# Kernel tuning notes

Measured on AMD Instinct MI355X. Metric: run time of the kernel, lower is better.

Reference implementation:

```python
import jax, jax.numpy as jnp
import numpy as np

N = 50000
E = 800000
D_IN = 128
D_HID = 128
D_OUT = 64
BN_EPS = 1e-5


def setup_inputs() -> dict:
    key = jax.random.key(0)
    ks = jax.random.split(key, 8)
    x = jax.random.normal(ks[0], (N, D_IN), dtype=jnp.float32)
    edge_index = jax.random.randint(ks[1], (2, E), 0, N, dtype=jnp.int64)
    # fc1
    W1 = jax.random.normal(ks[2], (D_IN, D_HID), dtype=jnp.float32) / np.sqrt(D_IN)
    b1 = jnp.zeros((D_HID,), dtype=jnp.float32)
    # bn1 affine params
    gamma = jnp.ones((D_HID,), dtype=jnp.float32)
    beta = jnp.zeros((D_HID,), dtype=jnp.float32)
    # fc2
    W2 = jax.random.normal(ks[3], (D_HID, D_OUT), dtype=jnp.float32) / np.sqrt(D_HID)
    b2 = jnp.zeros((D_OUT,), dtype=jnp.float32)
    return {"x": x, "W1": W1, "b1": b1, "gamma": gamma, "beta": beta,
            "W2": W2, "b2": b2, "edge_index": edge_index}


def _propagate(x, row, col):
    # add self loops for every node (reference convention)
    n = x.shape[0]
    sl = jnp.arange(n, dtype=row.dtype)
    row_f = jnp.concatenate([row, sl])
    col_f = jnp.concatenate([col, sl])
    # symmetric degree normalization: deg computed over destinations (col)
    deg = jax.ops.segment_sum(jnp.ones_like(col_f, dtype=x.dtype), col_f, num_segments=n)
    dis = deg ** -0.5
    w = dis[col_f] * dis[row_f]                       # [E+N]
    msg = w[:, None] * x[row_f]                       # [E+N, D] gather + scale
    return jax.ops.segment_sum(msg, col_f, num_segments=n)  # scatter-add


def reference(x, W1, b1, gamma, beta, W2, b2, edge_index):
    row, col = edge_index[0], edge_index[1]
    h = x @ W1 + b1                                   # [N, D_HID]
    h = _propagate(h, row, col)
    # BatchNorm1d with batch statistics (training-mode math, deterministic)
    mu = jnp.mean(h, axis=0)
    var = jnp.var(h, axis=0)
    h = (h - mu) * jax.lax.rsqrt(var + BN_EPS) * gamma + beta
    h = jax.nn.relu(h)
    # dropout treated as identity (eval) for a deterministic reference
    h = h @ W2 + b2                                   # [N, D_OUT]
    h = _propagate(h, row, col)
    return jax.nn.log_softmax(h, axis=1)
```

## Files before the change

### kernel.cpp

```cpp
#include <hip/hip_runtime.h>
#include <hip/hip_bf16.h>

#define N_NODES 50000
#define NE      800000
#define DIN     128
#define DHID    128
#define DOUT    64
#define BN_EPS  1e-5f
#define SLOT    64
#define NBUK    196
#define BCAP    4864
#define EPB     2048
#define NPART   32
#define LDW     132
#define LDW2    132

typedef __hip_bfloat16 bf16;
typedef short bf16x8 __attribute__((ext_vector_type(8)));
typedef float f32x4 __attribute__((ext_vector_type(4)));

__device__ __forceinline__ float ldf(const void* p, int i, int isbf) {
    if (isbf) return __bfloat162float(((const bf16*)p)[i]);
    return ((const float*)p)[i];
}
__device__ __forceinline__ unsigned short f2b(float f) {
    bf16 h = __float2bfloat16(f);
    return *(unsigned short*)&h;
}
__device__ __forceinline__ float2 up2(unsigned int u) {
    return make_float2(__uint_as_float(u << 16), __uint_as_float(u & 0xffff0000u));
}
__device__ __forceinline__ unsigned int pk2(float a, float b) {
    return ((unsigned int)f2b(a)) | (((unsigned int)f2b(b)) << 16);
}

#define DETECT_ISBF(W1raw, tid, sdet, isbf_out)                                   \
    if ((tid) == 0) sdet = 0;                                                     \
    __syncthreads();                                                              \
    {                                                                             \
        unsigned int u_ = ((unsigned int)((const unsigned short*)(W1raw))[tid]) << 16; \
        float f_ = fabsf(__uint_as_float(u_));                                    \
        if (!isnan(f_) && !isinf(f_) && f_ > 1e4f) atomicOr(&sdet, 1);            \
    }                                                                             \
    __syncthreads();                                                              \
    const int isbf_out = !sdet;

__global__ __launch_bounds__(256) void k_binA(const void* eiraw, int* __restrict__ gcnt,
                                              unsigned int* __restrict__ bpk) {
    __shared__ int hist4[4][256];
    __shared__ int cur4[4][256];
    __shared__ int eofs[256], gbase[256];
    __shared__ int wsum[4];
    __shared__ unsigned int stg[EPB];
    __shared__ int sdet;
    int tid = threadIdx.x;
    int lane = tid & 63;
    int wv = tid >> 6;
    if (tid == 0) sdet = 0;
    #pragma unroll
    for (int w2 = 0; w2 < 4; ++w2) hist4[w2][tid] = 0;
    __syncthreads();
    if (tid < 64 && ((const unsigned int*)eiraw)[2 * tid + 1] != 0u) atomicOr(&sdet, 1);
    __syncthreads();
    const int isll = !sdet;

    int e0 = blockIdx.x * EPB;
    int nE = NE - e0; if (nE > EPB) nE = EPB;
    int r[8], c[8];
    #pragma unroll
    for (int q = 0; q < 8; ++q) {
        int li = q * 256 + tid;
        if (li < nE) {
            int e = e0 + li;
            if (isll) { r[q] = (int)((const long long*)eiraw)[e]; c[q] = (int)((const long long*)eiraw)[NE + e]; }
            else      { r[q] = ((const int*)eiraw)[e];            c[q] = ((const int*)eiraw)[NE + e]; }
            atomicAdd(&hist4[wv][c[q] >> 8], 1);
        } else r[q] = -1;
    }
    __syncthreads();
    int h0 = hist4[0][tid], h1 = hist4[1][tid], h2 = hist4[2][tid], h3 = hist4[3][tid];
    int tot = h0 + h1 + h2 + h3;
    int inc = tot;
    #pragma unroll
    for (int off = 1; off < 64; off <<= 1) {
        int u = __shfl_up(inc, off, 64);
        if (lane >= off) inc += u;
    }
    if (lane == 63) wsum[wv] = inc;
    __syncthreads();
    int woff = 0;
    #pragma unroll
    for (int w2 = 0; w2 < 3; ++w2) if (w2 < wv) woff += wsum[w2];
    int ex = woff + inc - tot;
    eofs[tid] = ex;
    cur4[0][tid] = ex;
    cur4[1][tid] = ex + h0;
    cur4[2][tid] = ex + h0 + h1;
    cur4[3][tid] = ex + h0 + h1 + h2;
    if (tid < NBUK) gbase[tid] = atomicAdd(&gcnt[tid], tot);
    __syncthreads();
    #pragma unroll
    for (int q = 0; q < 8; ++q) {
        if (r[q] >= 0) {
            int b = c[q] >> 8;
            int p = atomicAdd(&cur4[wv][b], 1);
            stg[p] = ((unsigned int)b << 24) | ((unsigned int)(c[q] & 255) << 16) | (unsigned int)r[q];
        }
    }
    __syncthreads();
    for (int i = tid; i < nE; i += 256) {
        unsigned int v = stg[i];
        int b = v >> 24;
        int pos = gbase[b] + (i - eofs[b]);
        if (pos < BCAP) bpk[(size_t)b * BCAP + pos] = v;
    }
}

__global__ __launch_bounds__(256) void k_binB(const unsigned int* __restrict__ bpk, const int* __restrict__ gcnt,
                                              int* __restrict__ counts, int* __restrict__ ej) {
    __shared__ int cnt4[4][256];
    __shared__ int cur4[4][256];
    __shared__ int eofs[256];
    __shared__ int wsum[4];
    __shared__ unsigned int stg[BCAP];
    int b = blockIdx.x;
    int tid = threadIdx.x;
    int lane = tid & 63;
    int wv = tid >> 6;
    int m = gcnt[b]; if (m > BCAP) m = BCAP;
    #pragma unroll
    for (int w2 = 0; w2 < 4; ++w2) cnt4[w2][tid] = 0;
    __syncthreads();
    const unsigned int* src = bpk + (size_t)b * BCAP;
    for (int i = tid; i < m; i += 256)
        atomicAdd(&cnt4[wv][(src[i] >> 16) & 255], 1);
    __syncthreads();
    int h0 = cnt4[0][tid], h1 = cnt4[1][tid], h2 = cnt4[2][tid], h3 = cnt4[3][tid];
    int hv = h0 + h1 + h2 + h3;
    int inc = hv;
    #pragma unroll
    for (int off = 1; off < 64; off <<= 1) {
        int u = __shfl_up(inc, off, 64);
        if (lane >= off) inc += u;
    }
    if (lane == 63) wsum[wv] = inc;
    __syncthreads();
    int woff = 0;
    #pragma unroll
    for (int w2 = 0; w2 < 3; ++w2) if (w2 < wv) woff += wsum[w2];
    int ex = woff + inc - hv;
    eofs[tid] = ex;
    cur4[0][tid] = ex;
    cur4[1][tid] = ex + h0;
    cur4[2][tid] = ex + h0 + h1;
    cur4[3][tid] = ex + h0 + h1 + h2;
    int c0 = b << 8;
    int cg = c0 + tid;
    if (cg < N_NODES) {
        counts[cg] = hv;
        int hc = hv < SLOT ? hv : SLOT;
        int hp = (hc + 15) & ~15; if (hp > SLOT) hp = SLOT;
        for (int k = hc; k < hp; ++k) ej[(size_t)cg * SLOT + k] = N_NODES;
    }
    __syncthreads();
    for (int i = tid; i < m; i += 256) {
        unsigned int v = src[i];
        int cl = (v >> 16) & 255;
        int p = atomicAdd(&cur4[wv][cl], 1);
        stg[p] = v & 0x00ffffffu;
    }
    __syncthreads();
    for (int i = tid; i < m; i += 256) {
        unsigned int v = stg[i];
        int cl = v >> 16;
        int k = i - eofs[cl];
        if (k < SLOT) ej[(size_t)(c0 + cl) * SLOT + k] = (int)(v & 0xffffu);
    }
}

__global__ __launch_bounds__(256) void k_gemm1_mfma(const void* __restrict__ x, const void* __restrict__ W1,
                                                    const void* __restrict__ b1, const int* __restrict__ counts,
                                                    unsigned short* __restrict__ g1) {
    __shared__ unsigned short wt[128 * LDW];
    __shared__ int sdet;
    int tid = threadIdx.x;
    DETECT_ISBF(W1, tid, sdet, isbf)

    #pragma unroll 4
    for (int i = 0; i < 64; ++i) {
        int idx = i * 256 + tid;
        int k = idx >> 7, n = idx & 127;
        wt[n * LDW + k] = isbf ? ((const unsigned short*)W1)[idx]
                               : f2b(((const float*)W1)[idx]);
    }
    __syncthreads();

    int lane = tid & 63;
    int wave = tid >> 6;
    int m0 = blockIdx.x * 64 + wave * 16;
    int lm = lane & 15;
    int quad = lane >> 4;

    bf16x8 a[4];
    int arow = m0 + lm;
    int arow_c = arow < N_NODES ? arow : 0;
    if (isbf) {
        const unsigned short* xb = (const unsigned short*)x;
        #pragma unroll
        for (int q = 0; q < 4; ++q)
            a[q] = *(const bf16x8*)(xb + arow_c * DIN + q * 32 + quad * 8);
    } else {
        const float* xf = (const float*)x;
        #pragma unroll
        for (int q = 0; q < 4; ++q) {
            bf16x8 t;
            #pragma unroll
            for (int j = 0; j < 8; ++j)
                t[j] = (short)f2b(xf[arow_c * DIN + q * 32 + quad * 8 + j]);
            a[q] = t;
        }
    }

    float dsc[4];
    #pragma unroll
    for (int r = 0; r < 4; ++r) {
        int grow = m0 + quad * 4 + r;
        dsc[r] = (grow < N_NODES) ? rsqrtf((float)(counts[grow] + 1)) : 0.f;
    }

    #pragma unroll
    for (int nt = 0; nt < 8; ++nt) {
        int n0 = nt * 16;
        f32x4 acc = {0.f, 0.f, 0.f, 0.f};
        #pragma unroll
        for (int q = 0; q < 4; ++q) {
            bf16x8 b = *(const bf16x8*)(wt + (n0 + lm) * LDW + q * 32 + quad * 8);
            acc = __builtin_amdgcn_mfma_f32_16x16x32_bf16(a[q], b, acc, 0, 0, 0);
        }
        float bias = ldf(b1, n0 + lm, isbf);
        #pragma unroll
        for (int r = 0; r < 4; ++r) {
            int grow = m0 + quad * 4 + r;
            if (grow <= N_NODES)
                g1[grow * DHID + n0 + lm] = f2b(dsc[r] * (acc[r] + bias));
        }
    }
}

__global__ __launch_bounds__(256) void k_prop1(const int* __restrict__ counts, const int* __restrict__ ej,
                                               const unsigned int* __restrict__ g1p,
                                               unsigned int* __restrict__ agg1p,
                                               float* __restrict__ statsP) {
    __shared__ float sp[1024];
    int tid = threadIdx.x;
    int w = tid >> 6;
    int n = blockIdx.x * 4 + w;
    n = __builtin_amdgcn_readfirstlane(n);
    int lane = tid & 63;
    float ax = 0.f, ay = 0.f;
    if (n < N_NODES) {
        int cnt = counts[n];
        int t = cnt < SLOT ? cnt : SLOT;
        int tp = (t + 15) & ~15; if (tp > SLOT) tp = SLOT;
        const int* ejn = ej + (size_t)n * SLOT;
        float2 v = up2(g1p[(size_t)n * 64 + lane]);
        float ax0 = v.x, ay0 = v.y, ax1 = 0.f, ay1 = 0.f;
        float ax2 = 0.f, ay2 = 0.f, ax3 = 0.f, ay3 = 0.f;
        for (int j = 0; j < tp; j += 16) {
            const int4* ej4 = (const int4*)(ejn + j);
            int4 E0 = ej4[0], E1 = ej4[1], E2 = ej4[2], E3 = ej4[3];
            int e[16] = {E0.x, E0.y, E0.z, E0.w, E1.x, E1.y, E1.z, E1.w,
                         E2.x, E2.y, E2.z, E2.w, E3.x, E3.y, E3.z, E3.w};
            unsigned int gg[16];
            #pragma unroll
            for (int q = 0; q < 16; ++q) gg[q] = g1p[(size_t)e[q] * 64 + lane];
            #pragma unroll
            for (int q = 0; q < 16; ++q) {
                float2 f = up2(gg[q]);
                if ((q & 3) == 0) { ax0 += f.x; ay0 += f.y; }
                else if ((q & 3) == 1) { ax1 += f.x; ay1 += f.y; }
                else if ((q & 3) == 2) { ax2 += f.x; ay2 += f.y; }
                else { ax3 += f.x; ay3 += f.y; }
            }
        }
        float dv = rsqrtf((float)(cnt + 1));
        ax = dv * ((ax0 + ax1) + (ax2 + ax3));
        ay = dv * ((ay0 + ay1) + (ay2 + ay3));
        agg1p[(size_t)n * 64 + lane] = pk2(ax, ay);
    }
    sp[w * 256 + 2 * lane]       = ax;
    sp[w * 256 + 2 * lane + 1]   = ay;
    sp[w * 256 + 128 + 2 * lane] = ax * ax;
    sp[w * 256 + 129 + 2 * lane] = ay * ay;
    __syncthreads();
    float s = sp[tid] + sp[256 + tid] + sp[512 + tid] + sp[768 + tid];
    atomicAdd(&statsP[(blockIdx.x & (NPART - 1)) * 256 + tid], s);
}

__global__ __launch_bounds__(256) void k_gemm2_mfma(const unsigned int* __restrict__ agg1p,
                                                    const float* __restrict__ statsP,
                                                    const void* __restrict__ gamma, const void* __restrict__ beta,
                                                    const void* __restrict__ W2, const void* __restrict__ b2,
                                                    const void* __restrict__ W1, const int* __restrict__ counts,
                                                    unsigned short* __restrict__ g2) {
    __shared__ unsigned short w2t[64 * LDW2];
    __shared__ float sc[128], sh[128], redu[256];
    __shared__ int sdet;
    int tid = threadIdx.x;
    DETECT_ISBF(W1, tid, sdet, isbf)

    #pragma unroll 4
    for (int i = 0; i < 32; ++i) {
        int idx = i * 256 + tid;
        int k = idx >> 6, n = idx & 63;
        w2t[n * LDW2 + k] = isbf ? ((const unsigned short*)W2)[idx]
                                 : f2b(((const float*)W2)[idx]);
    }
    {
        float s = 0.f;
        #pragma unroll
        for (int p = 0; p < NPART; ++p) s += statsP[p * 256 + tid];
        redu[tid] = s;
    }
    __syncthreads();
    if (tid < 128) {
        const float invn = 1.0f / (float)N_NODES;
        float mu = redu[tid] * invn;
        float var = redu[128 + tid] * invn - mu * mu;
        float rs = rsqrtf(var + BN_EPS);
        float g = ldf(gamma, tid, isbf);
        sc[tid] = rs * g;
        sh[tid] = ldf(beta, tid, isbf) - mu * rs * g;
    }
    __syncthreads();

    int lane = tid & 63;
    int wave = tid >> 6;
    int m0 = blockIdx.x * 64 + wave * 16;
    int lm = lane & 15;
    int quad = lane >> 4;

    int arow = m0 + lm;
    int arow_c = arow < N_NODES ? arow : 0;
    bf16x8 a[4];
    #pragma unroll
    for (int q = 0; q < 4; ++q) {
        uint4 gv = *(const uint4*)(agg1p + (size_t)arow_c * 64 + q * 16 + quad * 4);
        int kb = q * 32 + quad * 8;
        float2 f0 = up2(gv.x), f1 = up2(gv.y), f2 = up2(gv.z), f3 = up2(gv.w);
        float e0 = f0.x * sc[kb + 0] + sh[kb + 0];
        float e1 = f0.y * sc[kb + 1] + sh[kb + 1];
        float e2 = f1.x * sc[kb + 2] + sh[kb + 2];
        float e3 = f1.y * sc[kb + 3] + sh[kb + 3];
        float e4 = f2.x * sc[kb + 4] + sh[kb + 4];
        float e5 = f2.y * sc[kb + 5] + sh[kb + 5];
        float e6 = f3.x * sc[kb + 6] + sh[kb + 6];
        float e7 = f3.y * sc[kb + 7] + sh[kb + 7];
        bf16x8 t;
        t[0] = (short)f2b(e0 > 0.f ? e0 : 0.f);
        t[1] = (short)f2b(e1 > 0.f ? e1 : 0.f);
        t[2] = (short)f2b(e2 > 0.f ? e2 : 0.f);
        t[3] = (short)f2b(e3 > 0.f ? e3 : 0.f);
        t[4] = (short)f2b(e4 > 0.f ? e4 : 0.f);
        t[5] = (short)f2b(e5 > 0.f ? e5 : 0.f);
        t[6] = (short)f2b(e6 > 0.f ? e6 : 0.f);
        t[7] = (short)f2b(e7 > 0.f ? e7 : 0.f);
        a[q] = t;
    }

    float dsc[4];
    #pragma unroll
    for (int r = 0; r < 4; ++r) {
        int grow = m0 + quad * 4 + r;
        dsc[r] = (grow < N_NODES) ? rsqrtf((float)(counts[grow] + 1)) : 0.f;
    }

    #pragma unroll
    for (int nt = 0; nt < 4; ++nt) {
        int n0 = nt * 16;
        f32x4 acc = {0.f, 0.f, 0.f, 0.f};
        #pragma unroll
        for (int q = 0; q < 4; ++q) {
            bf16x8 b = *(const bf16x8*)(w2t + (n0 + lm) * LDW2 + q * 32 + quad * 8);
            acc = __builtin_amdgcn_mfma_f32_16x16x32_bf16(a[q], b, acc, 0, 0, 0);
        }
        float bias = ldf(b2, n0 + lm, isbf);
        #pragma unroll
        for (int r = 0; r < 4; ++r) {
            int grow = m0 + quad * 4 + r;
            if (grow <= N_NODES)
                g2[grow * DOUT + n0 + lm] = f2b(dsc[r] * (acc[r] + bias));
        }
    }
}

__global__ __launch_bounds__(256) void k_prop2_lsm(const int* __restrict__ counts, const int* __restrict__ ej,
                                                   const unsigned int* __restrict__ g2p,
                                                   const void* __restrict__ W1, void* __restrict__ out) {
    __shared__ int sdet;
    int tid = threadIdx.x;
    DETECT_ISBF(W1, tid, sdet, isbf)

    int n = blockIdx.x * 8 + (tid >> 5);
    if (n >= N_NODES) return;
    int lane = tid & 31;
    int cnt = counts[n];
    int t = cnt < SLOT ? cnt : SLOT;
    int tp = (t + 15) & ~15; if (tp > SLOT) tp = SLOT;
    const int* ejn = ej + (size_t)n * SLOT;
    float2 v = up2(g2p[(size_t)n * 32 + lane]);
    float ax0 = v.x, ay0 = v.y, ax1 = 0.f, ay1 = 0.f;
    float ax2 = 0.f, ay2 = 0.f, ax3 = 0.f, ay3 = 0.f;
    for (int j = 0; j < tp; j += 16) {
        const int4* ej4 = (const int4*)(ejn + j);
        int4 E0 = ej4[0], E1 = ej4[1], E2 = ej4[2], E3 = ej4[3];
        int e[16] = {E0.x, E0.y, E0.z, E0.w, E1.x, E1.y, E1.z, E1.w,
                     E2.x, E2.y, E2.z, E2.w, E3.x, E3.y, E3.z, E3.w};
        unsigned int gg[16];
        #pragma unroll
        for (int q = 0; q < 16; ++q) gg[q] = g2p[(size_t)e[q] * 32 + lane];
        #pragma unroll
        for (int q = 0; q < 16; ++q) {
            float2 f = up2(gg[q]);
            if ((q & 3) == 0) { ax0 += f.x; ay0 += f.y; }
            else if ((q & 3) == 1) { ax1 += f.x; ay1 += f.y; }
            else if ((q & 3) == 2) { ax2 += f.x; ay2 += f.y; }
            else { ax3 += f.x; ay3 += f.y; }
        }
    }
    float dv = rsqrtf((float)(cnt + 1));
    float ax = dv * ((ax0 + ax1) + (ax2 + ax3));
    float ay = dv * ((ay0 + ay1) + (ay2 + ay3));
    float m = fmaxf(ax, ay);
    #pragma unroll
    for (int off = 16; off >= 1; off >>= 1) m = fmaxf(m, __shfl_xor(m, off, 32));
    float sum = __expf(ax - m) + __expf(ay - m);
    #pragma unroll
    for (int off = 16; off >= 1; off >>= 1) sum += __shfl_xor(sum, off, 32);
    float lse = m + __logf(sum);
    float rx = ax - lse, ry = ay - lse;
    if (isbf) {
        ((unsigned int*)out)[(size_t)n * 32 + lane] = pk2(rx, ry);
    } else {
        float2* o = (float2*)((float*)out + (size_t)n * 64 + 2 * lane);
        *o = make_float2(rx, ry);
    }
}

extern "C" void kernel_launch(void* const* d_in, const int* in_sizes, int n_in,
                              void* d_out, int out_size, void* d_ws, size_t ws_size,
                              hipStream_t stream) {
    const void* x     = d_in[0];
    const void* W1    = d_in[1];
    const void* b1    = d_in[2];
    const void* gamma = d_in[3];
    const void* beta  = d_in[4];
    const void* W2    = d_in[5];
    const void* b2    = d_in[6];
    const void* ei    = d_in[7];

    char* w = (char*)d_ws;
    float*          statsP = (float*)(w + 0);
    int*            gcnt   = (int*)(w + 32768);
    int*            counts = (int*)(w + 33792);
    int*            ej     = (int*)(w + 233792);
    unsigned int*   bpk    = (unsigned int*)(w + 13033792);
    unsigned short* g1     = (unsigned short*)(w + 16847168);
    unsigned int*   agg1p  = (unsigned int*)(w + 29647424);
    unsigned short* g2     = (unsigned short*)(w + 42447424);

    hipMemsetAsync(w, 0, 33792, stream);

    k_binA<<<(NE + EPB - 1) / EPB, 256, 0, stream>>>(ei, gcnt, bpk);
    k_binB<<<NBUK, 256, 0, stream>>>(bpk, gcnt, counts, ej);

    k_gemm1_mfma<<<(N_NODES + 63) / 64, 256, 0, stream>>>(x, W1, b1, counts, g1);

    k_prop1<<<(N_NODES + 3) / 4, 256, 0, stream>>>(counts, ej, (const unsigned int*)g1, agg1p, statsP);

    k_gemm2_mfma<<<(N_NODES + 63) / 64, 256, 0, stream>>>(agg1p, statsP, gamma, beta, W2, b2,
                                                          W1, counts, g2);

    k_prop2_lsm<<<(N_NODES + 7) / 8, 256, 0, stream>>>(counts, ej, (const unsigned int*)g2, W1, d_out);
}
```

Before: 216.9 us.

## Merge binning and first GEMM into one launch, apply source normalization in prop1

The bucket-sort second pass and the first MFMA GEMM now run as separate block ranges of a single kernel. This is possible because the GEMM no longer multiplies by the source degree normalization. That scaling moves into the first propagation, which gathers a per-node rsqrt(deg) array written by the binning blocks. The goal is to drop one launch and the dependency between binning and GEMM1 so both can overlap. The cost is an extra 4-byte gather per edge in prop1, and GEMM blocks must now wait behind the larger shared-memory footprint.

After: 213.8 us. No clear change (-1.5%).

```diff
diff --git a/kernel.cpp b/kernel.cpp
--- a/kernel.cpp
+++ b/kernel.cpp
@@ -14,6 +14,7 @@
 #define NPART   32
 #define LDW     132
 #define LDW2    132
+#define G1_BLOCKS ((N_NODES + 63) / 64)
 
 typedef __hip_bfloat16 bf16;
 typedef short bf16x8 __attribute__((ext_vector_type(8)));
@@ -116,138 +117,143 @@
     }
 }
 
-__global__ __launch_bounds__(256) void k_binB(const unsigned int* __restrict__ bpk, const int* __restrict__ gcnt,
-                                              int* __restrict__ counts, int* __restrict__ ej) {
-    __shared__ int cnt4[4][256];
-    __shared__ int cur4[4][256];
-    __shared__ int eofs[256];
-    __shared__ int wsum[4];
-    __shared__ unsigned int stg[BCAP];
-    int b = blockIdx.x;
-    int tid = threadIdx.x;
-    int lane = tid & 63;
-    int wv = tid >> 6;
-    int m = gcnt[b]; if (m > BCAP) m = BCAP;
-    #pragma unroll
-    for (int w2 = 0; w2 < 4; ++w2) cnt4[w2][tid] = 0;
-    __syncthreads();
-    const unsigned int* src = bpk + (size_t)b * BCAP;
-    for (int i = tid; i < m; i += 256)
-        atomicAdd(&cnt4[wv][(src[i] >> 16) & 255], 1);
-    __syncthreads();
-    int h0 = cnt4[0][tid], h1 = cnt4[1][tid], h2 = cnt4[2][tid], h3 = cnt4[3][tid];
-    int hv = h0 + h1 + h2 + h3;
-    int inc = hv;
-    #pragma unroll
-    for (int off = 1; off < 64; off <<= 1) {
-        int u = __shfl_up(inc, off, 64);
-        if (lane >= off) inc += u;
-    }
-    if (lane == 63) wsum[wv] = inc;
-    __syncthreads();
-    int woff = 0;
-    #pragma unroll
-    for (int w2 = 0; w2 < 3; ++w2) if (w2 < wv) woff += wsum[w2];
-    int ex = woff + inc - hv;
-    eofs[tid] = ex;
-    cur4[0][tid] = ex;
-    cur4[1][tid] = ex + h0;
-    cur4[2][tid] = ex + h0 + h1;
-    cur4[3][tid] = ex + h0 + h1 + h2;
-    int c0 = b << 8;
-    int cg = c0 + tid;
-    if (cg < N_NODES) {
-        counts[cg] = hv;
-        int hc = hv < SLOT ? hv : SLOT;
-        int hp = (hc + 15) & ~15; if (hp > SLOT) hp = SLOT;
-        for (int k = hc; k < hp; ++k) ej[(size_t)cg * SLOT + k] = N_NODES;
-    }
-    __syncthreads();
-    for (int i = tid; i < m; i += 256) {
-        unsigned int v = src[i];
-        int cl = (v >> 16) & 255;
-        int p = atomicAdd(&cur4[wv][cl], 1);
-        stg[p] = v & 0x00ffffffu;
-    }
-    __syncthreads();
-    for (int i = tid; i < m; i += 256) {
-        unsigned int v = stg[i];
-        int cl = v >> 16;
-        int k = i - eofs[cl];
-        if (k < SLOT) ej[(size_t)(c0 + cl) * SLOT + k] = (int)(v & 0xffffu);
-    }
-}
-
-__global__ __launch_bounds__(256) void k_gemm1_mfma(const void* __restrict__ x, const void* __restrict__ W1,
-                                                    const void* __restrict__ b1, const int* __restrict__ counts,
+__global__ __launch_bounds__(256) void k_binB_gemm1(const unsigned int* __restrict__ bpk,
+                                                    const int* __restrict__ gcnt,
+                                                    int* __restrict__ counts, float* __restrict__ disv,
+                                                    int* __restrict__ ej,
+                                                    const void* __restrict__ x, const void* __restrict__ W1,
+                                                    const void* __restrict__ b1,
                                                     unsigned short* __restrict__ g1) {
-    __shared__ unsigned short wt[128 * LDW];
+    __shared__ __align__(16) char smraw[33792];
     __shared__ int sdet;
     int tid = threadIdx.x;
-    DETECT_ISBF(W1, tid, sdet, isbf)
-
-    #pragma unroll 4
-    for (int i = 0; i < 64; ++i) {
-        int idx = i * 256 + tid;
-        int k = idx >> 7, n = idx & 127;
-        wt[n * LDW + k] = isbf ? ((const unsigned short*)W1)[idx]
-                               : f2b(((const float*)W1)[idx]);
-    }
-    __syncthreads();
-
-    int lane = tid & 63;
-    int wave = tid >> 6;
-    int m0 = blockIdx.x * 64 + wave * 16;
-    int lm = lane & 15;
-    int quad = lane >> 4;
-
-    bf16x8 a[4];
-    int arow = m0 + lm;
-    int arow_c = arow < N_NODES ? arow : 0;
-    if (isbf) {
-        const unsigned short* xb = (const unsigned short*)x;
-        #pragma unroll
-        for (int q = 0; q < 4; ++q)
-            a[q] = *(const bf16x8*)(xb + arow_c * DIN + q * 32 + quad * 8);
+
+    if (blockIdx.x < NBUK) {
+        int (*cnt4)[256] = (int(*)[256])smraw;
+        int (*cur4)[256] = (int(*)[256])(smraw + 4096);
+        int* eofs        = (int*)(smraw + 8192);
+        int* wsum        = (int*)(smraw + 9216);
+        unsigned int* stg = (unsigned int*)(smraw + 9232);
+
+        int b = blockIdx.x;
+        int lane = tid & 63;
+        int wv = tid >> 6;
+        int m = gcnt[b]; if (m > BCAP) m = BCAP;
+        #pragma unroll
+        for (int w2 = 0; w2 < 4; ++w2) cnt4[w2][tid] = 0;
+        __syncthreads();
+        const unsigned int* src = bpk + (size_t)b * BCAP;
+        for (int i = tid; i < m; i += 256)
+            atomicAdd(&cnt4[wv][(src[i] >> 16) & 255], 1);
+        __syncthreads();
+        int h0 = cnt4[0][tid], h1 = cnt4[1][tid], h2 = cnt4[2][tid], h3 = cnt4[3][tid];
+        int hv = h0 + h1 + h2 + h3;
+        int inc = hv;
+        #pragma unroll
+        for (int off = 1; off < 64; off <<= 1) {
+            int u = __shfl_up(inc, off, 64);
+            if (lane >= off) inc += u;
+        }
+        if (lane == 63) wsum[wv] = inc;
+        __syncthreads();
+        int woff = 0;
+        #pragma unroll
+        for (int w2 = 0; w2 < 3; ++w2) if (w2 < wv) woff += wsum[w2];
+        int ex = woff + inc - hv;
+        eofs[tid] = ex;
+        cur4[0][tid] = ex;
+        cur4[1][tid] = ex + h0;
+        cur4[2][tid] = ex + h0 + h1;
+        cur4[3][tid] = ex + h0 + h1 + h2;
+        int c0 = b << 8;
+        int cg = c0 + tid;
+        if (cg < N_NODES) {
+            counts[cg] = hv;
+            disv[cg] = rsqrtf((float)(hv + 1));
+            int hc = hv < SLOT ? hv : SLOT;
+            int hp = (hc + 15) & ~15; if (hp > SLOT) hp = SLOT;
+            for (int k = hc; k < hp; ++k) ej[(size_t)cg * SLOT + k] = N_NODES;
+        } else if (cg == N_NODES) {
+            disv[cg] = 0.f;
+        }
+        __syncthreads();
+        for (int i = tid; i < m; i += 256) {
+            unsigned int v = src[i];
+            int cl = (v >> 16) & 255;
+            int p = atomicAdd(&cur4[wv][cl], 1);
+            stg[p] = v & 0x00ffffffu;
+        }
+        __syncthreads();
+        for (int i = tid; i < m; i += 256) {
+            unsigned int v = stg[i];
+            int cl = v >> 16;
+            int k = i - eofs[cl];
+            if (k < SLOT) ej[(size_t)(c0 + cl) * SLOT + k] = (int)(v & 0xffffu);
+        }
     } else {
-        const float* xf = (const float*)x;
-        #pragma unroll
-        for (int q = 0; q < 4; ++q) {
-            bf16x8 t;
-            #pragma unroll
-            for (int j = 0; j < 8; ++j)
-                t[j] = (short)f2b(xf[arow_c * DIN + q * 32 + quad * 8 + j]);
-            a[q] = t;
-        }
-    }
-
-    float dsc[4];
-    #pragma unroll
-    for (int r = 0; r < 4; ++r) {
-        int grow = m0 + quad * 4 + r;
-        dsc[r] = (grow < N_NODES) ? rsqrtf((float)(counts[grow] + 1)) : 0.f;
-    }
-
-    #pragma unroll
-    for (int nt = 0; nt < 8; ++nt) {
-        int n0 = nt * 16;
-        f32x4 acc = {0.f, 0.f, 0.f, 0.f};
-        #pragma unroll
-        for (int q = 0; q < 4; ++q) {
-            bf16x8 b = *(const bf16x8*)(wt + (n0 + lm) * LDW + q * 32 + quad * 8);
-            acc = __builtin_amdgcn_mfma_f32_16x16x32_bf16(a[q], b, acc, 0, 0, 0);
-        }
-        float bias = ldf(b1, n0 + lm, isbf);
-        #pragma unroll
-        for (int r = 0; r < 4; ++r) {
-            int grow = m0 + quad * 4 + r;
-            if (grow <= N_NODES)
-                g1[grow * DHID + n0 + lm] = f2b(dsc[r] * (acc[r] + bias));
-        }
-    }
-}
-
-__global__ __launch_bounds__(256) void k_prop1(const int* __restrict__ counts, const int* __restrict__ ej,
+        unsigned short* wt = (unsigned short*)smraw;
+        DETECT_ISBF(W1, tid, sdet, isbf)
+
+        #pragma unroll 4
+        for (int i = 0; i < 64; ++i) {
+            int idx = i * 256 + tid;
+            int k = idx >> 7, n = idx & 127;
+            wt[n * LDW + k] = isbf ? ((const unsigned short*)W1)[idx]
+                                   : f2b(((const float*)W1)[idx]);
+        }
+        __syncthreads();
+
+        int lane = tid & 63;
+        int wave = tid >> 6;
+        int bid = blockIdx.x - NBUK;
+        int m0 = bid * 64 + wave * 16;
+        int lm = lane & 15;
+        int quad = lane >> 4;
+
+        bf16x8 a[4];
+        int arow = m0 + lm;
+        int arow_c = arow < N_NODES ? arow : 0;
+        if (isbf) {
+            const unsigned short* xb = (const unsigned short*)x;
+            #pragma unroll
+            for (int q = 0; q < 4; ++q)
+                a[q] = *(const bf16x8*)(xb + arow_c * DIN + q * 32 + quad * 8);
+        } else {
+            const float* xf = (const float*)x;
+            #pragma unroll
+            for (int q = 0; q < 4; ++q) {
+                bf16x8 t;
+                #pragma unroll
+                for (int j = 0; j < 8; ++j)
+                    t[j] = (short)f2b(xf[arow_c * DIN + q * 32 + quad * 8 + j]);
+                a[q] = t;
+            }
+        }
+
+        #pragma unroll
+        for (int nt = 0; nt < 8; ++nt) {
+            int n0 = nt * 16;
+            f32x4 acc = {0.f, 0.f, 0.f, 0.f};
+            #pragma unroll
+            for (int q = 0; q < 4; ++q) {
+                bf16x8 b = *(const bf16x8*)(wt + (n0 + lm) * LDW + q * 32 + quad * 8);
+                acc = __builtin_amdgcn_mfma_f32_16x16x32_bf16(a[q], b, acc, 0, 0, 0);
+            }
+            float bias = ldf(b1, n0 + lm, isbf);
+            #pragma unroll
+            for (int r = 0; r < 4; ++r) {
+                int grow = m0 + quad * 4 + r;
+                if (grow <= N_NODES) {
+                    float val = (grow < N_NODES) ? (acc[r] + bias) : 0.f;
+                    g1[grow * DHID + n0 + lm] = f2b(val);
+                }
+            }
+        }
+    }
+}
+
+__global__ __launch_bounds__(256) void k_prop1(const int* __restrict__ counts, const float* __restrict__ disv,
+                                               const int* __restrict__ ej,
                                                const unsigned int* __restrict__ g1p,
                                                unsigned int* __restrict__ agg1p,
                                                float* __restrict__ statsP) {
@@ -260,11 +266,12 @@
     float ax = 0.f, ay = 0.f;
     if (n < N_NODES) {
         int cnt = counts[n];
+        float dv = disv[n];
         int t = cnt < SLOT ? cnt : SLOT;
         int tp = (t + 15) & ~15; if (tp > SLOT) tp = SLOT;
         const int* ejn = ej + (size_t)n * SLOT;
         float2 v = up2(g1p[(size_t)n * 64 + lane]);
-        float ax0 = v.x, ay0 = v.y, ax1 = 0.f, ay1 = 0.f;
+        float ax0 = dv * v.x, ay0 = dv * v.y, ax1 = 0.f, ay1 = 0.f;
         float ax2 = 0.f, ay2 = 0.f, ax3 = 0.f, ay3 = 0.f;
         for (int j = 0; j < tp; j += 16) {
             const int4* ej4 = (const int4*)(ejn + j);
@@ -272,18 +279,18 @@
             int e[16] = {E0.x, E0.y, E0.z, E0.w, E1.x, E1.y, E1.z, E1.w,
                          E2.x, E2.y, E2.z, E2.w, E3.x, E3.y, E3.z, E3.w};
             unsigned int gg[16];
-            #pragma unroll
-            for (int q = 0; q < 16; ++q) gg[q] = g1p[(size_t)e[q] * 64 + lane];
+            float ds[16];
+            #pragma unroll
+            for (int q = 0; q < 16; ++q) { gg[q] = g1p[(size_t)e[q] * 64 + lane]; ds[q] = disv[e[q]]; }
             #pragma unroll
             for (int q = 0; q < 16; ++q) {
                 float2 f = up2(gg[q]);
-                if ((q & 3) == 0) { ax0 += f.x; ay0 += f.y; }
-                else if ((q & 3) == 1) { ax1 += f.x; ay1 += f.y; }
-                else if ((q & 3) == 2) { ax2 += f.x; ay2 += f.y; }
-                else { ax3 += f.x; ay3 += f.y; }
+                if ((q & 3) == 0) { ax0 = fmaf(ds[q], f.x, ax0); ay0 = fmaf(ds[q], f.y, ay0); }
+                else if ((q & 3) == 1) { ax1 = fmaf(ds[q], f.x, ax1); ay1 = fmaf(ds[q], f.y, ay1); }
+                else if ((q & 3) == 2) { ax2 = fmaf(ds[q], f.x, ax2); ay2 = fmaf(ds[q], f.y, ay2); }
+                else { ax3 = fmaf(ds[q], f.x, ax3); ay3 = fmaf(ds[q], f.y, ay3); }
             }
         }
-        float dv = rsqrtf((float)(cnt + 1));
         ax = dv * ((ax0 + ax1) + (ax2 + ax3));
         ay = dv * ((ay0 + ay1) + (ay2 + ay3));
         agg1p[(size_t)n * 64 + lane] = pk2(ax, ay);
@@ -463,20 +470,20 @@
     float*          statsP = (float*)(w + 0);
     int*            gcnt   = (int*)(w + 32768);
     int*            counts = (int*)(w + 33792);
-    int*            ej     = (int*)(w + 233792);
-    unsigned int*   bpk    = (unsigned int*)(w + 13033792);
-    unsigned short* g1     = (unsigned short*)(w + 16847168);
-    unsigned int*   agg1p  = (unsigned int*)(w + 29647424);
-    unsigned short* g2     = (unsigned short*)(w + 42447424);
+    float*          disv   = (float*)(w + 233792);
+    int*            ej     = (int*)(w + 433808);
+    unsigned int*   bpk    = (unsigned int*)(w + 13233808);
+    unsigned short* g1     = (unsigned short*)(w + 17047184);
+    unsigned int*   agg1p  = (unsigned int*)(w + 29847440);
+    unsigned short* g2     = (unsigned short*)(w + 42647440);
 
     hipMemsetAsync(w, 0, 33792, stream);
 
     k_binA<<<(NE + EPB - 1) / EPB, 256, 0, stream>>>(ei, gcnt, bpk);
-    k_binB<<<NBUK, 256, 0, stream>>>(bpk, gcnt, counts, ej);
-
-    k_gemm1_mfma<<<(N_NODES + 63) / 64, 256, 0, stream>>>(x, W1, b1, counts, g1);
-
-    k_prop1<<<(N_NODES + 3) / 4, 256, 0, stream>>>(counts, ej, (const unsigned int*)g1, agg1p, statsP);
+
+    k_binB_gemm1<<<NBUK + G1_BLOCKS, 256, 0, stream>>>(bpk, gcnt, counts, disv, ej, x, W1, b1, g1);
+
+    k_prop1<<<(N_NODES + 3) / 4, 256, 0, stream>>>(counts, disv, ej, (const unsigned int*)g1, agg1p, statsP);
 
     k_gemm2_mfma<<<(N_NODES + 63) / 64, 256, 0, stream>>>(agg1p, statsP, gamma, beta, W2, b2,
                                                           W1, counts, g2);
```
